# Kernel tuning notes

Measured on AMD Instinct MI355X. Metric: run time of the kernel, lower is better.

## Reference

```python
import jax, jax.numpy as jnp
import numpy as np

N_NODES = 8192
N_EDGES = 262144
IN_F, HID, OUT_F = 512, 512, 256


def setup_inputs() -> dict:
    key = jax.random.key(0)
    k_x, k_e, k_w1, k_b1, k_w2, k_b2 = jax.random.split(key, 6)
    x = jax.random.normal(k_x, (N_NODES, IN_F), dtype=jnp.float32)
    edge_index = jax.random.randint(k_e, (2, N_EDGES), 0, N_NODES, dtype=jnp.int64)
    # xavier-uniform linear weights, stored as [in, out]
    def xavier(k, fan_in, fan_out):
        lim = np.sqrt(6.0 / (fan_in + fan_out)).astype(np.float32)
        return jax.random.uniform(k, (fan_in, fan_out), jnp.float32, -lim, lim)
    W1 = xavier(k_w1, IN_F, HID)
    b1 = jax.random.uniform(k_b1, (HID,), jnp.float32, -0.05, 0.05)
    W2 = xavier(k_w2, HID, OUT_F)
    b2 = jax.random.uniform(k_b2, (OUT_F,), jnp.float32, -0.05, 0.05)
    return {"x": x, "edge_index": edge_index, "W1": W1, "b1": b1, "W2": W2, "b2": b2}


def _gcn_layer(x, edge_index, W, b):
    # H' = D~^{-1/2} A~ D~^{-1/2} H W + b, with A~ = A + I
    n = x.shape[0]
    adj = jnp.zeros((n, n), dtype=x.dtype).at[edge_index[0], edge_index[1]].set(1.0)
    adj = adj + jnp.eye(n, dtype=x.dtype)
    degree = jnp.clip(adj.sum(axis=1), 1.0, None)
    d_inv_sqrt = degree ** -0.5
    adj_norm = adj * d_inv_sqrt[None, :] * d_inv_sqrt[:, None]
    return (adj_norm @ x) @ W + b


def reference(x, edge_index, W1, b1, W2, b2):
    h = jax.nn.relu(_gcn_layer(x, edge_index, W1, b1))
    # dropout p=0.0 -> identity
    out = _gcn_layer(h, edge_index, W2, b2)
    return out
```

## Files before the change

kernel.cpp:

```cpp
#include <hip/hip_runtime.h>
#include <hip/hip_bf16.h>
#include <stdint.h>

#define N_NODES 8192
#define N_EDGES 262144
#define IN_F 512
#define HID 512
#define OUT_F 256
#define CAP 128

typedef __attribute__((ext_vector_type(8))) short short8;
typedef __attribute__((ext_vector_type(4))) float f32x4;

__device__ __forceinline__ float bflo(unsigned int u) {
  union { unsigned int x; float f; } c; c.x = u << 16; return c.f;
}
__device__ __forceinline__ float bfhi(unsigned int u) {
  union { unsigned int x; float f; } c; c.x = u & 0xffff0000u; return c.f;
}
__device__ __forceinline__ unsigned short f2bf(float f) {
  union { float f; unsigned int u; } c; c.f = f;
  unsigned int r = c.u + 0x7fffu + ((c.u >> 16) & 1u);
  return (unsigned short)(r >> 16);
}

__device__ __forceinline__ void gload_lds16(const void* g, void* l) {
  __builtin_amdgcn_global_load_lds((const __attribute__((address_space(1))) void*)g,
                                   (__attribute__((address_space(3))) void*)l, 16, 0, 0);
}

__global__ __launch_bounds__(256) void build_adj(
    const int* __restrict__ ei, unsigned int* __restrict__ bitmap,
    int* __restrict__ cnt, int* __restrict__ adj) {
  int e = blockIdx.x * blockDim.x + threadIdx.x;
  if (e >= N_EDGES) return;
  int i = ei[e];
  int j = ei[N_EDGES + e];
  int lin = i * N_NODES + j;
  unsigned int bit = 1u << (lin & 31);
  unsigned int old = atomicOr(&bitmap[lin >> 5], bit);
  if (!(old & bit)) {
    int p = atomicAdd(&cnt[i], 1);
    if (p < CAP) adj[i * CAP + p] = j;
  }
}

__global__ __launch_bounds__(256) void cvt_bf16_vec(
    const float* __restrict__ in, unsigned short* __restrict__ out, int n4) {
  int idx = blockIdx.x * blockDim.x + threadIdx.x;
  if (idx >= n4) return;
  const float4 v = ((const float4*)in)[idx];
  uint2 o;
  o.x = (unsigned int)f2bf(v.x) | ((unsigned int)f2bf(v.y) << 16);
  o.y = (unsigned int)f2bf(v.z) | ((unsigned int)f2bf(v.w) << 16);
  ((uint2*)out)[idx] = o;
}

__global__ __launch_bounds__(256) void prep_weights(
    const float* __restrict__ W1, const float* __restrict__ W2,
    unsigned short* __restrict__ W1t, unsigned short* __restrict__ W2t) {
  int idx = blockIdx.x * blockDim.x + threadIdx.x;
  if (idx < IN_F * HID) {
    int k = idx >> 9, n = idx & 511;
    W1t[n * IN_F + k] = f2bf(W1[idx]);
  } else {
    int r = idx - IN_F * HID;
    if (r < HID * OUT_F) {
      int k = r >> 8, n = r & 255;
      W2t[n * HID + k] = f2bf(W2[r]);
    }
  }
}

template<int BM, int BN>
__global__ __launch_bounds__(256) void gemm_bt(
    const unsigned short* __restrict__ A, const unsigned short* __restrict__ Bt,
    unsigned short* __restrict__ C, int M, int N, int K) {
  constexpr int MR = BM / 32, NR = BN / 32;
  __shared__ __align__(16) unsigned short As[BM * 64];
  __shared__ __align__(16) unsigned short Bs[BN * 64];
  const int tid = threadIdx.x;
  const long row0 = (long)blockIdx.x * BM;
  const long col0 = (long)blockIdx.y * BN;
  const int lane = tid & 63;
  const int wid = tid >> 6;
  const int ln15 = lane & 15, hi = lane >> 4;
  const int wr = (wid >> 1) * (BM / 2), wc = (wid & 1) * (BN / 2);
  const int sr = tid >> 3;
  const int sk = (tid & 7) * 8;
  f32x4 acc[MR][NR] = {};

  for (int k0 = 0; k0 < K; k0 += 64) {
#pragma unroll
    for (int c = 0; c < MR; ++c)
      gload_lds16(A  + (row0 + c * 32 + sr) * (long)K + k0 + sk, &As[(c * 256 + tid) * 8]);
#pragma unroll
    for (int c = 0; c < NR; ++c)
      gload_lds16(Bt + (col0 + c * 32 + sr) * (long)K + k0 + sk, &Bs[(c * 256 + tid) * 8]);
    __syncthreads();
#pragma unroll
    for (int kk = 0; kk < 64; kk += 32) {
      short8 a[MR], b[NR];
#pragma unroll
      for (int m = 0; m < MR; ++m)
        a[m] = *(const short8*)&As[(wr + m * 16 + ln15) * 64 + kk + hi * 8];
#pragma unroll
      for (int n = 0; n < NR; ++n)
        b[n] = *(const short8*)&Bs[(wc + n * 16 + ln15) * 64 + kk + hi * 8];
#pragma unroll
      for (int m = 0; m < MR; ++m)
#pragma unroll
        for (int n = 0; n < NR; ++n)
          acc[m][n] = __builtin_amdgcn_mfma_f32_16x16x32_bf16(a[m], b[n], acc[m][n], 0, 0, 0);
    }
    __syncthreads();
  }
#pragma unroll
  for (int m = 0; m < MR; ++m)
#pragma unroll
    for (int n = 0; n < NR; ++n)
#pragma unroll
      for (int r = 0; r < 4; ++r) {
        long row = row0 + wr + m * 16 + hi * 4 + r;
        long col = col0 + wc + n * 16 + ln15;
        C[row * N + col] = f2bf(acc[m][n][r]);
      }
}

__global__ __launch_bounds__(256) void aggregate_relu(
    const unsigned short* __restrict__ T, const int* __restrict__ cnt,
    const int* __restrict__ adj, const float* __restrict__ bias,
    unsigned short* __restrict__ H) {
  const int i = blockIdx.x;
  const int tid = threadIdx.x;
  const int lane = tid & 63, w = tid >> 6;
  __shared__ int js[CAP];
  __shared__ float ws[CAP];
  __shared__ float part[4][512];
  int n = cnt[i]; if (n > CAP) n = CAP;
  if (tid < n) { int j = adj[i * CAP + tid]; js[tid] = j; ws[tid] = rsqrtf((float)(cnt[j] + 1)); }
  __syncthreads();
  float a[8] = {};
  for (int e = w; e < n; e += 4) {
    const uint4 v = *(const uint4*)&T[(long)js[e] * 512 + lane * 8];
    float wj = ws[e];
    a[0] += wj * bflo(v.x); a[1] += wj * bfhi(v.x);
    a[2] += wj * bflo(v.y); a[3] += wj * bfhi(v.y);
    a[4] += wj * bflo(v.z); a[5] += wj * bfhi(v.z);
    a[6] += wj * bflo(v.w); a[7] += wj * bfhi(v.w);
  }
  *(float4*)&part[w][lane * 8]     = make_float4(a[0], a[1], a[2], a[3]);
  *(float4*)&part[w][lane * 8 + 4] = make_float4(a[4], a[5], a[6], a[7]);
  __syncthreads();
  const float di = rsqrtf((float)(cnt[i] + 1));
  unsigned int u = *(const unsigned int*)&T[(long)i * 512 + tid * 2];
  float s0 = part[0][2*tid]   + part[1][2*tid]   + part[2][2*tid]   + part[3][2*tid]   + di * bflo(u);
  float s1 = part[0][2*tid+1] + part[1][2*tid+1] + part[2][2*tid+1] + part[3][2*tid+1] + di * bfhi(u);
  const float2 bb = *(const float2*)&bias[2 * tid];
  float h0 = fmaxf(di * s0 + bb.x, 0.f);
  float h1 = fmaxf(di * s1 + bb.y, 0.f);
  *(unsigned int*)&H[(long)i * 512 + tid * 2] =
      (unsigned int)f2bf(h0) | ((unsigned int)f2bf(h1) << 16);
}

__global__ __launch_bounds__(256) void aggregate_out(
    const unsigned short* __restrict__ T, const int* __restrict__ cnt,
    const int* __restrict__ adj, const float* __restrict__ bias,
    float* __restrict__ out) {
  const int i = blockIdx.x;
  const int tid = threadIdx.x;
  const int lane = tid & 63, w = tid >> 6;
  __shared__ int js[CAP];
  __shared__ float ws[CAP];
  __shared__ float part[4][256];
  int n = cnt[i]; if (n > CAP) n = CAP;
  if (tid < n) { int j = adj[i * CAP + tid]; js[tid] = j; ws[tid] = rsqrtf((float)(cnt[j] + 1)); }
  __syncthreads();
  float a[4] = {};
  for (int e = w; e < n; e += 4) {
    const uint2 v = *(const uint2*)&T[(long)js[e] * 256 + lane * 4];
    float wj = ws[e];
    a[0] += wj * bflo(v.x); a[1] += wj * bfhi(v.x);
    a[2] += wj * bflo(v.y); a[3] += wj * bfhi(v.y);
  }
  *(float4*)&part[w][lane * 4] = make_float4(a[0], a[1], a[2], a[3]);
  __syncthreads();
  const float di = rsqrtf((float)(cnt[i] + 1));
  float self = di * __uint_as_float(((unsigned int)T[(long)i * 256 + tid]) << 16);
  float s = part[0][tid] + part[1][tid] + part[2][tid] + part[3][tid] + self;
  out[(long)i * 256 + tid] = di * s + bias[tid];
}

extern "C" void kernel_launch(void* const* d_in, const int* in_sizes, int n_in,
                              void* d_out, int out_size, void* d_ws, size_t ws_size,
                              hipStream_t stream) {
  const float* x  = (const float*)d_in[0];
  const int*   ei = (const int*)d_in[1];
  const float* W1 = (const float*)d_in[2];
  const float* b1 = (const float*)d_in[3];
  const float* W2 = (const float*)d_in[4];
  const float* b2 = (const float*)d_in[5];
  float* out = (float*)d_out;

  char* ws = (char*)d_ws;
  unsigned int* bitmap = (unsigned int*)ws;  ws += 8388608;
  int* cnt   = (int*)ws;                     ws += 32768;
  int* adj   = (int*)ws;                     ws += (size_t)N_NODES * CAP * 4;
  unsigned short* Xb  = (unsigned short*)ws; ws += (size_t)N_NODES * IN_F * 2;
  unsigned short* W1t = (unsigned short*)ws; ws += (size_t)IN_F * HID * 2;
  unsigned short* W2t = (unsigned short*)ws; ws += (size_t)HID * OUT_F * 2;
  unsigned short* T1  = (unsigned short*)ws; ws += (size_t)N_NODES * HID * 2;
  unsigned short* H   = (unsigned short*)ws; ws += (size_t)N_NODES * HID * 2;
  unsigned short* T2  = (unsigned short*)ws; ws += (size_t)N_NODES * OUT_F * 2;

  hipMemsetAsync(bitmap, 0, 8388608 + 32768, stream);

  build_adj<<<N_EDGES / 256, 256, 0, stream>>>(ei, bitmap, cnt, adj);

  cvt_bf16_vec<<<N_NODES * IN_F / 4 / 256, 256, 0, stream>>>(x, Xb, N_NODES * IN_F / 4);
  prep_weights<<<(IN_F * HID + HID * OUT_F) / 256, 256, 0, stream>>>(W1, W2, W1t, W2t);

  gemm_bt<128, 64><<<dim3(N_NODES / 128, HID / 64), 256, 0, stream>>>(Xb, W1t, T1, N_NODES, HID, IN_F);
  aggregate_relu<<<N_NODES, 256, 0, stream>>>(T1, cnt, adj, b1, H);

  gemm_bt<64, 64><<<dim3(N_NODES / 64, OUT_F / 64), 256, 0, stream>>>(H, W2t, T2, N_NODES, OUT_F, HID);
  aggregate_out<<<N_NODES, 256, 0, stream>>>(T2, cnt, adj, b2, out);
}
```

Before: 175.1 us.

## Replace bitmap dedup with per-node dedup, fuse prep kernels, split aggregate columns

Drops the 8 MB dense bitmap and its memset. Edges are appended to per-node lists without dedup, then a per-node kernel removes duplicates in shared memory and precomputes inverse-sqrt degrees. The conversion, weight transpose and edge scatter are fused into one launch, and the first aggregation is split across two column halves to double the grid. This removes a large memset and the scattered atomics on the bitmap, but raw duplicate edges now count toward the CAP of 128 before dedup, and the quadratic per-node dedup adds a launch.

```diff
diff --git a/kernel.cpp b/kernel.cpp
--- a/kernel.cpp
+++ b/kernel.cpp
@@ -18,6 +18,9 @@
 __device__ __forceinline__ float bfhi(unsigned int u) {
   union { unsigned int x; float f; } c; c.x = u & 0xffff0000u; return c.f;
 }
+__device__ __forceinline__ float bf1(unsigned short s) {
+  union { unsigned int x; float f; } c; c.x = (unsigned int)s << 16; return c.f;
+}
 __device__ __forceinline__ unsigned short f2bf(float f) {
   union { float f; unsigned int u; } c; c.f = f;
   unsigned int r = c.u + 0x7fffu + ((c.u >> 16) & 1u);
@@ -29,46 +32,66 @@
                                    (__attribute__((address_space(3))) void*)l, 16, 0, 0);
 }
 
-__global__ __launch_bounds__(256) void build_adj(
-    const int* __restrict__ ei, unsigned int* __restrict__ bitmap,
-    int* __restrict__ cnt, int* __restrict__ adj) {
-  int e = blockIdx.x * blockDim.x + threadIdx.x;
-  if (e >= N_EDGES) return;
-  int i = ei[e];
-  int j = ei[N_EDGES + e];
-  int lin = i * N_NODES + j;
-  unsigned int bit = 1u << (lin & 31);
-  unsigned int old = atomicOr(&bitmap[lin >> 5], bit);
-  if (!(old & bit)) {
+#define NB_CVT  4096
+#define NB_W1   1024
+#define NB_W2    512
+#define NB_EDGE 1024
+__global__ __launch_bounds__(256) void prep_all(
+    const float* __restrict__ x, const float* __restrict__ W1, const float* __restrict__ W2,
+    const int* __restrict__ ei,
+    unsigned short* __restrict__ Xb, unsigned short* __restrict__ W1t,
+    unsigned short* __restrict__ W2t, int* __restrict__ cnt, int* __restrict__ adj) {
+  const int b = blockIdx.x, tid = threadIdx.x;
+  if (b < NB_CVT) {
+    int idx = b * 256 + tid;
+    const float4 v = ((const float4*)x)[idx];
+    uint2 o;
+    o.x = (unsigned int)f2bf(v.x) | ((unsigned int)f2bf(v.y) << 16);
+    o.y = (unsigned int)f2bf(v.z) | ((unsigned int)f2bf(v.w) << 16);
+    ((uint2*)Xb)[idx] = o;
+  } else if (b < NB_CVT + NB_W1) {
+    int idx = (b - NB_CVT) * 256 + tid;
+    int k = idx >> 9, n = idx & 511;
+    W1t[n * IN_F + k] = f2bf(W1[idx]);
+  } else if (b < NB_CVT + NB_W1 + NB_W2) {
+    int idx = (b - NB_CVT - NB_W1) * 256 + tid;
+    int k = idx >> 8, n = idx & 255;
+    W2t[n * HID + k] = f2bf(W2[idx]);
+  } else {
+    int e = (b - NB_CVT - NB_W1 - NB_W2) * 256 + tid;
+    int i = ei[e];
+    int j = ei[N_EDGES + e];
     int p = atomicAdd(&cnt[i], 1);
     if (p < CAP) adj[i * CAP + p] = j;
   }
 }
 
-__global__ __launch_bounds__(256) void cvt_bf16_vec(
-    const float* __restrict__ in, unsigned short* __restrict__ out, int n4) {
-  int idx = blockIdx.x * blockDim.x + threadIdx.x;
-  if (idx >= n4) return;
-  const float4 v = ((const float4*)in)[idx];
-  uint2 o;
-  o.x = (unsigned int)f2bf(v.x) | ((unsigned int)f2bf(v.y) << 16);
-  o.y = (unsigned int)f2bf(v.z) | ((unsigned int)f2bf(v.w) << 16);
-  ((uint2*)out)[idx] = o;
-}
-
-__global__ __launch_bounds__(256) void prep_weights(
-    const float* __restrict__ W1, const float* __restrict__ W2,
-    unsigned short* __restrict__ W1t, unsigned short* __restrict__ W2t) {
-  int idx = blockIdx.x * blockDim.x + threadIdx.x;
-  if (idx < IN_F * HID) {
-    int k = idx >> 9, n = idx & 511;
-    W1t[n * IN_F + k] = f2bf(W1[idx]);
-  } else {
-    int r = idx - IN_F * HID;
-    if (r < HID * OUT_F) {
-      int k = r >> 8, n = r & 255;
-      W2t[n * HID + k] = f2bf(W2[r]);
-    }
+__global__ __launch_bounds__(128) void dedup_node(
+    int* __restrict__ cnt, int* __restrict__ adj, float* __restrict__ dis) {
+  const int i = blockIdx.x, t = threadIdx.x;
+  __shared__ int js[CAP];
+  __shared__ unsigned char keep[CAP];
+  int n0 = cnt[i]; if (n0 > CAP) n0 = CAP;
+  if (t < n0) js[t] = adj[i * CAP + t];
+  __syncthreads();
+  bool k = false;
+  if (t < n0) {
+    k = true;
+    int jt = js[t];
+    for (int s = 0; s < t; ++s) if (js[s] == jt) { k = false; break; }
+  }
+  keep[t] = k;
+  __syncthreads();
+  if (k) {
+    int r = 0;
+    for (int s = 0; s < t; ++s) r += keep[s];
+    adj[i * CAP + r] = js[t];
+  }
+  if (t == 0) {
+    int nd = 0;
+    for (int s = 0; s < n0; ++s) nd += keep[s];
+    cnt[i] = nd;
+    dis[i] = rsqrtf((float)(nd + 1));
   }
 }
 
@@ -129,52 +152,46 @@
 
 __global__ __launch_bounds__(256) void aggregate_relu(
     const unsigned short* __restrict__ T, const int* __restrict__ cnt,
-    const int* __restrict__ adj, const float* __restrict__ bias,
-    unsigned short* __restrict__ H) {
+    const int* __restrict__ adj, const float* __restrict__ dis,
+    const float* __restrict__ bias, unsigned short* __restrict__ H) {
   const int i = blockIdx.x;
+  const int c0 = blockIdx.y * 256;
   const int tid = threadIdx.x;
   const int lane = tid & 63, w = tid >> 6;
   __shared__ int js[CAP];
   __shared__ float ws[CAP];
-  __shared__ float part[4][512];
-  int n = cnt[i]; if (n > CAP) n = CAP;
-  if (tid < n) { int j = adj[i * CAP + tid]; js[tid] = j; ws[tid] = rsqrtf((float)(cnt[j] + 1)); }
-  __syncthreads();
-  float a[8] = {};
+  __shared__ float part[4][256];
+  int n = cnt[i];
+  if (tid < n) { int j = adj[i * CAP + tid]; js[tid] = j; ws[tid] = dis[j]; }
+  __syncthreads();
+  float a[4] = {};
   for (int e = w; e < n; e += 4) {
-    const uint4 v = *(const uint4*)&T[(long)js[e] * 512 + lane * 8];
+    const uint2 v = *(const uint2*)&T[(long)js[e] * 512 + c0 + lane * 4];
     float wj = ws[e];
     a[0] += wj * bflo(v.x); a[1] += wj * bfhi(v.x);
     a[2] += wj * bflo(v.y); a[3] += wj * bfhi(v.y);
-    a[4] += wj * bflo(v.z); a[5] += wj * bfhi(v.z);
-    a[6] += wj * bflo(v.w); a[7] += wj * bfhi(v.w);
-  }
-  *(float4*)&part[w][lane * 8]     = make_float4(a[0], a[1], a[2], a[3]);
-  *(float4*)&part[w][lane * 8 + 4] = make_float4(a[4], a[5], a[6], a[7]);
-  __syncthreads();
-  const float di = rsqrtf((float)(cnt[i] + 1));
-  unsigned int u = *(const unsigned int*)&T[(long)i * 512 + tid * 2];
-  float s0 = part[0][2*tid]   + part[1][2*tid]   + part[2][2*tid]   + part[3][2*tid]   + di * bflo(u);
-  float s1 = part[0][2*tid+1] + part[1][2*tid+1] + part[2][2*tid+1] + part[3][2*tid+1] + di * bfhi(u);
-  const float2 bb = *(const float2*)&bias[2 * tid];
-  float h0 = fmaxf(di * s0 + bb.x, 0.f);
-  float h1 = fmaxf(di * s1 + bb.y, 0.f);
-  *(unsigned int*)&H[(long)i * 512 + tid * 2] =
-      (unsigned int)f2bf(h0) | ((unsigned int)f2bf(h1) << 16);
+  }
+  *(float4*)&part[w][lane * 4] = make_float4(a[0], a[1], a[2], a[3]);
+  __syncthreads();
+  const float di = dis[i];
+  float self = di * bf1(T[(long)i * 512 + c0 + tid]);
+  float s = part[0][tid] + part[1][tid] + part[2][tid] + part[3][tid] + self;
+  float h = fmaxf(di * s + bias[c0 + tid], 0.f);
+  H[(long)i * 512 + c0 + tid] = f2bf(h);
 }
 
 __global__ __launch_bounds__(256) void aggregate_out(
     const unsigned short* __restrict__ T, const int* __restrict__ cnt,
-    const int* __restrict__ adj, const float* __restrict__ bias,
-    float* __restrict__ out) {
+    const int* __restrict__ adj, const float* __restrict__ dis,
+    const float* __restrict__ bias, float* __restrict__ out) {
   const int i = blockIdx.x;
   const int tid = threadIdx.x;
   const int lane = tid & 63, w = tid >> 6;
   __shared__ int js[CAP];
   __shared__ float ws[CAP];
   __shared__ float part[4][256];
-  int n = cnt[i]; if (n > CAP) n = CAP;
-  if (tid < n) { int j = adj[i * CAP + tid]; js[tid] = j; ws[tid] = rsqrtf((float)(cnt[j] + 1)); }
+  int n = cnt[i];
+  if (tid < n) { int j = adj[i * CAP + tid]; js[tid] = j; ws[tid] = dis[j]; }
   __syncthreads();
   float a[4] = {};
   for (int e = w; e < n; e += 4) {
@@ -185,8 +202,8 @@
   }
   *(float4*)&part[w][lane * 4] = make_float4(a[0], a[1], a[2], a[3]);
   __syncthreads();
-  const float di = rsqrtf((float)(cnt[i] + 1));
-  float self = di * __uint_as_float(((unsigned int)T[(long)i * 256 + tid]) << 16);
+  const float di = dis[i];
+  float self = di * bf1(T[(long)i * 256 + tid]);
   float s = part[0][tid] + part[1][tid] + part[2][tid] + part[3][tid] + self;
   out[(long)i * 256 + tid] = di * s + bias[tid];
 }
@@ -203,9 +220,9 @@
   float* out = (float*)d_out;
 
   char* ws = (char*)d_ws;
-  unsigned int* bitmap = (unsigned int*)ws;  ws += 8388608;
   int* cnt   = (int*)ws;                     ws += 32768;
   int* adj   = (int*)ws;                     ws += (size_t)N_NODES * CAP * 4;
+  float* dis = (float*)ws;                   ws += 32768;
   unsigned short* Xb  = (unsigned short*)ws; ws += (size_t)N_NODES * IN_F * 2;
   unsigned short* W1t = (unsigned short*)ws; ws += (size_t)IN_F * HID * 2;
   unsigned short* W2t = (unsigned short*)ws; ws += (size_t)HID * OUT_F * 2;
@@ -213,16 +230,15 @@
   unsigned short* H   = (unsigned short*)ws; ws += (size_t)N_NODES * HID * 2;
   unsigned short* T2  = (unsigned short*)ws; ws += (size_t)N_NODES * OUT_F * 2;
 
-  hipMemsetAsync(bitmap, 0, 8388608 + 32768, stream);
-
-  build_adj<<<N_EDGES / 256, 256, 0, stream>>>(ei, bitmap, cnt, adj);
-
-  cvt_bf16_vec<<<N_NODES * IN_F / 4 / 256, 256, 0, stream>>>(x, Xb, N_NODES * IN_F / 4);
-  prep_weights<<<(IN_F * HID + HID * OUT_F) / 256, 256, 0, stream>>>(W1, W2, W1t, W2t);
+  hipMemsetAsync(cnt, 0, 32768, stream);
+
+  prep_all<<<NB_CVT + NB_W1 + NB_W2 + NB_EDGE, 256, 0, stream>>>(
+      x, W1, W2, ei, Xb, W1t, W2t, cnt, adj);
+  dedup_node<<<N_NODES, 128, 0, stream>>>(cnt, adj, dis);
 
   gemm_bt<128, 64><<<dim3(N_NODES / 128, HID / 64), 256, 0, stream>>>(Xb, W1t, T1, N_NODES, HID, IN_F);
-  aggregate_relu<<<N_NODES, 256, 0, stream>>>(T1, cnt, adj, b1, H);
+  aggregate_relu<<<dim3(N_NODES, 2), 256, 0, stream>>>(T1, cnt, adj, dis, b1, H);
 
   gemm_bt<64, 64><<<dim3(N_NODES / 64, OUT_F / 64), 256, 0, stream>>>(H, W2t, T2, N_NODES, OUT_F, HID);
-  aggregate_out<<<N_NODES, 256, 0, stream>>>(T2, cnt, adj, b2, out);
-}
+  aggregate_out<<<N_NODES, 256, 0, stream>>>(T2, cnt, adj, dis, b2, out);
+}
```

Measured after the change: 183.0 us. +4.5%, slower.
